# Optimization experiments

Measured on AMD Instinct MI355X. Metric: run time of the kernel, lower is better.

## Reference

```python
import jax, jax.numpy as jnp
import numpy as np


def _gcn_conv(x, W, b, src, dst, num_nodes):
    """PyG GCNConv: linear transform, add self-loops, symmetric norm, scatter-add."""
    h = x @ W  # [N, out] - transform first (cheaper gather on small dim)
    loop = jnp.arange(num_nodes, dtype=src.dtype)
    s = jnp.concatenate([src, loop])  # sources (message senders)
    d = jnp.concatenate([dst, loop])  # targets (aggregators)
    deg = jax.ops.segment_sum(jnp.ones_like(d, dtype=h.dtype), d, num_segments=num_nodes)
    dinv = jnp.where(deg > 0, jax.lax.rsqrt(deg), 0.0)
    norm = dinv[s] * dinv[d]  # [E+N]
    msg = h[s] * norm[:, None]  # gather + scale
    out = jax.ops.segment_sum(msg, d, num_segments=num_nodes)  # scatter-add
    return out + b


def setup_inputs() -> dict:
    key = jax.random.key(0)
    k1, k2, k3, k4 = jax.random.split(key, 4)
    N, F_IN, H, C, E = 100000, 128, 16, 7, 3200000
    x = jax.random.normal(k1, (N, F_IN), dtype=jnp.float32)
    edge_index = jax.random.randint(k2, (2, E), 0, N, dtype=jnp.int64)
    W1 = jax.random.normal(k3, (F_IN, H), dtype=jnp.float32) / np.sqrt(F_IN)
    b1 = jnp.zeros((H,), dtype=jnp.float32)
    W2 = jax.random.normal(k4, (H, C), dtype=jnp.float32) / np.sqrt(H)
    b2 = jnp.zeros((C,), dtype=jnp.float32)
    return {"x": x, "edge_index": edge_index, "W1": W1, "b1": b1, "W2": W2, "b2": b2}


def reference(x, edge_index, W1, b1, W2, b2):
    N = x.shape[0]
    src, dst = edge_index[0], edge_index[1]
    h = _gcn_conv(x, W1, b1, src, dst, N)
    h = jax.nn.relu(h)
    # dropout is identity in eval mode
    h = _gcn_conv(h, W2, b2, src, dst, N)
    return jax.nn.log_softmax(h, axis=1)
```

## Files before the change

kernel.cpp:

```cpp
#include <hip/hip_runtime.h>

#define BSHIFT 7
#define BNODES 128
#define BMASK 127
#define CAP 6144
#define PT 512
#define P_EPB (PT * 16)
#define TPB 256

__device__ __forceinline__ unsigned pkbf2(float a, float b) {
    unsigned ua = __float_as_uint(a), ub = __float_as_uint(b);
    ua = (ua + 0x7fffu + ((ua >> 16) & 1u)) >> 16;
    ub = (ub + 0x7fffu + ((ub >> 16) & 1u)) >> 16;
    return ua | (ub << 16);
}
__device__ __forceinline__ float bflo(unsigned u) { return __uint_as_float(u << 16); }
__device__ __forceinline__ float bfhi(unsigned u) { return __uint_as_float(u & 0xffff0000u); }

__global__ void detect_kernel(const unsigned int* __restrict__ w, int* __restrict__ flag,
                              int* __restrict__ gcur, int nb) {
    __shared__ int any;
    if (threadIdx.x == 0) any = 0;
    __syncthreads();
    int nz = 0;
    for (int k = threadIdx.x; k < 1024; k += blockDim.x)
        if (w[2 * k + 1] != 0u) nz = 1;
    if (nz) atomicOr(&any, 1);
    for (int i = threadIdx.x; i < nb; i += blockDim.x) gcur[i] = 0;
    __syncthreads();
    if (threadIdx.x == 0) *flag = (any == 0) ? 1 : 0;
}

__global__ __launch_bounds__(PT) void fused_place_gemm_kernel(
    const void* __restrict__ ei, const int* __restrict__ flag,
    int* __restrict__ gcur, unsigned* __restrict__ pairs,
    const float* __restrict__ x, const float* __restrict__ W1,
    float* __restrict__ hs, int E, int nb, int pb, int N) {
    __shared__ alignas(16) char smem[47120];
    int tid = threadIdx.x;
    if ((int)blockIdx.x < pb) {
        int* cnt  = (int*)smem;
        int* bbs  = (int*)(smem + 4096);
        int* cur  = (int*)(smem + 8208);
        int* ssum = (int*)(smem + 12304);
        unsigned* stage = (unsigned*)(smem + 14352);
        const bool is64 = (*flag != 0);
        const long long* e64 = (const long long*)ei;
        const int* e32 = (const int*)ei;
        int e0 = blockIdx.x * P_EPB;
        int tot = E - e0; if (tot > P_EPB) tot = P_EPB;
        for (int b = tid; b < nb; b += PT) cnt[b] = 0;
        __syncthreads();
        unsigned pk[16];
        int bk[16];
#pragma unroll
        for (int k = 0; k < 16; ++k) {
            int i = tid + k * PT;
            bk[k] = -1;
            if (i < tot) {
                int e = e0 + i;
                int s, d;
                if (is64) { s = (int)e64[e]; d = (int)e64[E + e]; }
                else      { s = e32[e];      d = e32[E + e]; }
                int b = d >> BSHIFT;
                bk[k] = b;
                pk[k] = ((unsigned)s << BSHIFT) | (unsigned)(d & BMASK);
                atomicAdd(&cnt[b], 1);
            }
        }
        __syncthreads();
        int t2 = tid * 2;
        int c0 = (t2 < nb) ? cnt[t2] : 0;
        int c1 = (t2 + 1 < nb) ? cnt[t2 + 1] : 0;
        int ts = c0 + c1;
        ssum[tid] = ts;
        __syncthreads();
        for (int off = 1; off < PT; off <<= 1) {
            int v = (tid >= off) ? ssum[tid - off] : 0;
            __syncthreads();
            ssum[tid] += v;
            __syncthreads();
        }
        int excl = ssum[tid] - ts;
        if (tid == PT - 1) bbs[nb] = ssum[PT - 1];
        int gb0 = 0, gb1 = 0;
        if (t2 < nb && c0) gb0 = atomicAdd(&gcur[t2], c0);
        if (t2 + 1 < nb && c1) gb1 = atomicAdd(&gcur[t2 + 1], c1);
        if (t2 < nb)     { bbs[t2] = excl;          cnt[t2] = gb0;     cur[t2] = 0; }
        if (t2 + 1 < nb) { bbs[t2 + 1] = excl + c0; cnt[t2 + 1] = gb1; cur[t2 + 1] = 0; }
        __syncthreads();
#pragma unroll
        for (int k = 0; k < 16; ++k) {
            if (bk[k] >= 0) {
                int r = atomicAdd(&cur[bk[k]], 1);
                stage[bbs[bk[k]] + r] = pk[k];
            }
        }
        __syncthreads();
        for (int i = tid; i < tot; i += PT) {
            int lo = 0, hi = nb;
            while (hi - lo > 1) { int mid = (lo + hi) >> 1; if (bbs[mid] <= i) lo = mid; else hi = mid; }
            int slot = cnt[lo] + (i - bbs[lo]);
            if (slot < CAP) pairs[(size_t)lo * CAP + slot] = stage[i];
        }
    } else {
        float* Ws = (float*)smem;
        for (int i = tid; i < 2048; i += PT) Ws[i] = W1[i];
        __syncthreads();
        int n = ((int)blockIdx.x - pb) * PT + tid;
        if (n >= N) return;
        const float4* xp = (const float4*)(x + (size_t)n * 128);
        float a[16];
#pragma unroll
        for (int j = 0; j < 16; ++j) a[j] = 0.f;
#pragma unroll 4
        for (int k4 = 0; k4 < 32; ++k4) {
            float4 xv = xp[k4];
            const float* wr = &Ws[k4 * 64];
#pragma unroll
            for (int j = 0; j < 16; ++j) a[j] += xv.x * wr[j];
#pragma unroll
            for (int j = 0; j < 16; ++j) a[j] += xv.y * wr[16 + j];
#pragma unroll
            for (int j = 0; j < 16; ++j) a[j] += xv.z * wr[32 + j];
#pragma unroll
            for (int j = 0; j < 16; ++j) a[j] += xv.w * wr[48 + j];
        }
        float4* hp = (float4*)(hs + (size_t)n * 16);
#pragma unroll
        for (int j4 = 0; j4 < 4; ++j4) {
            float4 v;
            v.x = a[j4 * 4 + 0]; v.y = a[j4 * 4 + 1];
            v.z = a[j4 * 4 + 2]; v.w = a[j4 * 4 + 3];
            hp[j4] = v;
        }
    }
}

__global__ __launch_bounds__(1024) void scanb_kernel(const int* __restrict__ gcur,
                                                     int* __restrict__ bbase, int nb) {
    __shared__ int sh[1024];
    int t = threadIdx.x;
    int v = 0;
    if (t < nb) { v = gcur[t]; if (v > CAP) v = CAP; }
    sh[t] = v;
    __syncthreads();
    for (int off = 1; off < 1024; off <<= 1) {
        int u = (t >= off) ? sh[t - off] : 0;
        __syncthreads();
        sh[t] += u;
        __syncthreads();
    }
    if (t < nb) bbase[t] = sh[t] - v;
}

__global__ __launch_bounds__(TPB) void csr_build_kernel(
    const unsigned* __restrict__ pairs, const int* __restrict__ gcur,
    const int* __restrict__ bbase, int* __restrict__ csr,
    int* __restrict__ row, int* __restrict__ degA,
    const float* __restrict__ hs1f, uint4* __restrict__ hs1b, int N) {
    __shared__ int hist[BNODES];
    __shared__ int sc[BNODES];
    __shared__ int cur[BNODES];
    __shared__ int stage[CAP];
    int tid = threadIdx.x;
    int b = blockIdx.x;
    if (tid < BNODES) hist[tid] = 0;
    __syncthreads();
    int cnt = gcur[b]; if (cnt > CAP) cnt = CAP;
    int base = bbase[b];
    const unsigned* sl = pairs + (size_t)b * CAP;
    for (int i = tid; i < cnt; i += TPB)
        atomicAdd(&hist[sl[i] & BMASK], 1);
    __syncthreads();
    if (tid < BNODES) sc[tid] = hist[tid];
    __syncthreads();
    for (int off = 1; off < BNODES; off <<= 1) {
        int u = (tid < BNODES && tid >= off) ? sc[tid - off] : 0;
        __syncthreads();
        if (tid < BNODES) sc[tid] += u;
        __syncthreads();
    }
    if (tid < BNODES) {
        int excl = sc[tid] - hist[tid];
        sc[tid] = excl;
        cur[tid] = 0;
        int node = (b << BSHIFT) + tid;
        if (node < N) {
            row[node]  = base + excl;
            degA[node] = hist[tid];
        }
    }
    __syncthreads();
    for (int i = tid; i < cnt; i += TPB) {
        unsigned val = sl[i];
        int l = val & BMASK;
        int r = atomicAdd(&cur[l], 1);
        stage[sc[l] + r] = (int)(val >> BSHIFT);
    }
    __syncthreads();
    for (int i = tid; i < cnt; i += TPB)
        csr[base + i] = stage[i];
    int nodeBase = b << BSHIFT;
    {
        int ln = tid >> 1, half = tid & 1;
        int node = nodeBase + ln;
        if (node < N) {
            float s = rsqrtf((float)(hist[ln] + 1));
            const float4* F = (const float4*)(hs1f + (size_t)node * 16);
            float4 f0 = F[half * 2], f1 = F[half * 2 + 1];
            uint4 u;
            u.x = pkbf2(f0.x * s, f0.y * s); u.y = pkbf2(f0.z * s, f0.w * s);
            u.z = pkbf2(f1.x * s, f1.y * s); u.w = pkbf2(f1.z * s, f1.w * s);
            hs1b[(size_t)node * 2 + half] = u;
        }
    }
}

__global__ __launch_bounds__(TPB) void agg1_kernel(
    const uint4* __restrict__ hs1b, const int* __restrict__ csr,
    const int* __restrict__ row, const int* __restrict__ degA,
    const float* __restrict__ W2, const float* __restrict__ b1,
    uint4* __restrict__ hs2b, int N) {
    __shared__ float Ws[112];
    __shared__ float bs[16];
    int tid = threadIdx.x;
    if (tid < 112) Ws[tid] = W2[tid];
    if (tid < 16) bs[tid] = b1[tid];
    __syncthreads();
    int g = blockIdx.x * TPB + tid;
    int n = g >> 2, quarter = g & 3;
    int st = 0, cnt = 0;
    if (n < N) { st = row[n]; cnt = degA[n]; }
    float acc[16];
#pragma unroll
    for (int j = 0; j < 16; ++j) acc[j] = 0.f;
    int i = st + quarter, end = st + cnt;
    for (; i + 4 < end; i += 8) {
        int s0 = csr[i], s1 = csr[i + 4];
        uint4 g0 = hs1b[(size_t)s0 * 2], g1 = hs1b[(size_t)s0 * 2 + 1];
        uint4 h0 = hs1b[(size_t)s1 * 2], h1 = hs1b[(size_t)s1 * 2 + 1];
        acc[0]  += bflo(g0.x) + bflo(h0.x); acc[1]  += bfhi(g0.x) + bfhi(h0.x);
        acc[2]  += bflo(g0.y) + bflo(h0.y); acc[3]  += bfhi(g0.y) + bfhi(h0.y);
        acc[4]  += bflo(g0.z) + bflo(h0.z); acc[5]  += bfhi(g0.z) + bfhi(h0.z);
        acc[6]  += bflo(g0.w) + bflo(h0.w); acc[7]  += bfhi(g0.w) + bfhi(h0.w);
        acc[8]  += bflo(g1.x) + bflo(h1.x); acc[9]  += bfhi(g1.x) + bfhi(h1.x);
        acc[10] += bflo(g1.y) + bflo(h1.y); acc[11] += bfhi(g1.y) + bfhi(h1.y);
        acc[12] += bflo(g1.z) + bflo(h1.z); acc[13] += bfhi(g1.z) + bfhi(h1.z);
        acc[14] += bflo(g1.w) + bflo(h1.w); acc[15] += bfhi(g1.w) + bfhi(h1.w);
    }
    if (i < end) {
        int s0 = csr[i];
        uint4 g0 = hs1b[(size_t)s0 * 2], g1 = hs1b[(size_t)s0 * 2 + 1];
        acc[0]  += bflo(g0.x); acc[1]  += bfhi(g0.x);
        acc[2]  += bflo(g0.y); acc[3]  += bfhi(g0.y);
        acc[4]  += bflo(g0.z); acc[5]  += bfhi(g0.z);
        acc[6]  += bflo(g0.w); acc[7]  += bfhi(g0.w);
        acc[8]  += bflo(g1.x); acc[9]  += bfhi(g1.x);
        acc[10] += bflo(g1.y); acc[11] += bfhi(g1.y);
        acc[12] += bflo(g1.z); acc[13] += bfhi(g1.z);
        acc[14] += bflo(g1.w); acc[15] += bfhi(g1.w);
    }
#pragma unroll
    for (int j = 0; j < 16; ++j) {
        acc[j] += __shfl_xor(acc[j], 1);
        acc[j] += __shfl_xor(acc[j], 2);
    }
    if (quarter == 0 && n < N) {
        float sc = rsqrtf((float)(cnt + 1));
        uint4 sA = hs1b[(size_t)n * 2], sB = hs1b[(size_t)n * 2 + 1];
        float self[16] = {bflo(sA.x), bfhi(sA.x), bflo(sA.y), bfhi(sA.y),
                          bflo(sA.z), bfhi(sA.z), bflo(sA.w), bfhi(sA.w),
                          bflo(sB.x), bfhi(sB.x), bflo(sB.y), bfhi(sB.y),
                          bflo(sB.z), bfhi(sB.z), bflo(sB.w), bfhi(sB.w)};
        float v[16];
#pragma unroll
        for (int j = 0; j < 16; ++j)
            v[j] = fmaxf(0.f, sc * (acc[j] + self[j]) + bs[j]);
        float h[7];
#pragma unroll
        for (int j = 0; j < 7; ++j) h[j] = 0.f;
#pragma unroll
        for (int k = 0; k < 16; ++k)
#pragma unroll
            for (int j = 0; j < 7; ++j) h[j] += v[k] * Ws[k * 7 + j];
        uint4 u;
        u.x = pkbf2(h[0] * sc, h[1] * sc);
        u.y = pkbf2(h[2] * sc, h[3] * sc);
        u.z = pkbf2(h[4] * sc, h[5] * sc);
        u.w = pkbf2(h[6] * sc, 0.f);
        hs2b[n] = u;
    }
}

__global__ __launch_bounds__(TPB) void agg2_kernel(
    const uint4* __restrict__ hs2b, const int* __restrict__ csr,
    const int* __restrict__ row, const int* __restrict__ degA,
    const float* __restrict__ b2, float* __restrict__ out, int N) {
    __shared__ float bs[8];
    if (threadIdx.x < 7) bs[threadIdx.x] = b2[threadIdx.x];
    __syncthreads();
    int g = blockIdx.x * TPB + threadIdx.x;
    int n = g >> 2, quarter = g & 3;
    int st = 0, cnt = 0;
    if (n < N) { st = row[n]; cnt = degA[n]; }
    float acc[7];
#pragma unroll
    for (int j = 0; j < 7; ++j) acc[j] = 0.f;
    int i = st + quarter, end = st + cnt;
    for (; i + 4 < end; i += 8) {
        int s0 = csr[i], s1 = csr[i + 4];
        uint4 q = hs2b[s0];
        uint4 r = hs2b[s1];
        acc[0] += bflo(q.x) + bflo(r.x); acc[1] += bfhi(q.x) + bfhi(r.x);
        acc[2] += bflo(q.y) + bflo(r.y); acc[3] += bfhi(q.y) + bfhi(r.y);
        acc[4] += bflo(q.z) + bflo(r.z); acc[5] += bfhi(q.z) + bfhi(r.z);
        acc[6] += bflo(q.w) + bflo(r.w);
    }
    if (i < end) {
        uint4 q = hs2b[csr[i]];
        acc[0] += bflo(q.x); acc[1] += bfhi(q.x);
        acc[2] += bflo(q.y); acc[3] += bfhi(q.y);
        acc[4] += bflo(q.z); acc[5] += bfhi(q.z);
        acc[6] += bflo(q.w);
    }
#pragma unroll
    for (int j = 0; j < 7; ++j) {
        acc[j] += __shfl_xor(acc[j], 1);
        acc[j] += __shfl_xor(acc[j], 2);
    }
    if (quarter == 0 && n < N) {
        float sc = rsqrtf((float)(cnt + 1));
        uint4 q = hs2b[n];
        float self[7] = {bflo(q.x), bfhi(q.x), bflo(q.y), bfhi(q.y),
                         bflo(q.z), bfhi(q.z), bflo(q.w)};
        float v[7];
#pragma unroll
        for (int j = 0; j < 7; ++j)
            v[j] = sc * (acc[j] + self[j]) + bs[j];
        float m = v[0];
#pragma unroll
        for (int j = 1; j < 7; ++j) m = fmaxf(m, v[j]);
        float ssum = 0.f;
#pragma unroll
        for (int j = 0; j < 7; ++j) ssum += __expf(v[j] - m);
        float l = m + __logf(ssum);
        float* op = out + (size_t)n * 7;
#pragma unroll
        for (int j = 0; j < 7; ++j) op[j] = v[j] - l;
    }
}

extern "C" void kernel_launch(void* const* d_in, const int* in_sizes, int n_in,
                              void* d_out, int out_size, void* d_ws, size_t ws_size,
                              hipStream_t stream) {
    const float* x  = (const float*)d_in[0];
    const void*  ei = d_in[1];
    const float* W1 = (const float*)d_in[2];
    const float* b1 = (const float*)d_in[3];
    const float* W2 = (const float*)d_in[4];
    const float* b2 = (const float*)d_in[5];
    float* out = (float*)d_out;

    const int Hh  = in_sizes[3];
    const int Fin = in_sizes[2] / Hh;
    const int N   = in_sizes[0] / Fin;
    const long long twoE = in_sizes[1];
    const int E = (int)(twoE / 2);
    const int nb = (N + BNODES - 1) >> BSHIFT;
    (void)n_in; (void)out_size; (void)ws_size;

    char* p = (char*)d_ws;
    auto alloc = [&](size_t bytes) {
        char* r = p;
        p += (bytes + 63) & ~(size_t)63;
        return r;
    };
    int*      flag  = (int*)alloc(sizeof(int));
    int*      gcur  = (int*)alloc(sizeof(int) * (size_t)nb);
    int*      bbase = (int*)alloc(sizeof(int) * 1024);
    unsigned* pairs = (unsigned*)alloc(sizeof(unsigned) * (size_t)nb * CAP);
    int*      csr   = (int*)alloc(sizeof(int) * (size_t)E);
    int*      rowA  = (int*)alloc(sizeof(int) * (size_t)N);
    int*      degA  = (int*)alloc(sizeof(int) * (size_t)N);
    float*    hs1f  = (float*)alloc(sizeof(float) * (size_t)N * 16);
    uint4*    hs1b  = (uint4*)alloc(32 * (size_t)N);
    uint4*    hs2b  = (uint4*)alloc(16 * (size_t)N);

    const int pb = (E + P_EPB - 1) / P_EPB;
    const int gb = (N + PT - 1) / PT;

    detect_kernel<<<1, 256, 0, stream>>>((const unsigned int*)ei, flag, gcur, nb);
    fused_place_gemm_kernel<<<pb + gb, PT, 0, stream>>>(
        ei, flag, gcur, pairs, x, W1, hs1f, E, nb, pb, N);
    scanb_kernel<<<1, 1024, 0, stream>>>(gcur, bbase, nb);
    csr_build_kernel<<<nb, TPB, 0, stream>>>(pairs, gcur, bbase, csr, rowA, degA, hs1f, hs1b, N);
    int aggBlk = (4 * N + TPB - 1) / TPB;
    agg1_kernel<<<aggBlk, TPB, 0, stream>>>(hs1b, csr, rowA, degA, W2, b1, hs2b, N);
    agg2_kernel<<<aggBlk, TPB, 0, stream>>>(hs2b, csr, rowA, degA, b2, out, N);
}
```

Before: 119.7 us.

## Drop bucket scan kernel, store GEMM output as bf16, use 8 lanes per node

Removes the single-block scan kernel by giving each CSR bucket a fixed CAP-sized slot (base = b*CAP), so the scan launch and its serialization go away. The first GEMM now writes bf16-packed outputs instead of fp32, which halves that intermediate's write and read traffic. The normalization step then re-rounds to bf16, adding a second rounding. Both aggregation kernels use 8 threads per node instead of 4, with one more shuffle stage, to expose more memory parallelism per node.

```diff
diff --git a/kernel.cpp b/kernel.cpp
--- a/kernel.cpp
+++ b/kernel.cpp
@@ -35,7 +35,7 @@
     const void* __restrict__ ei, const int* __restrict__ flag,
     int* __restrict__ gcur, unsigned* __restrict__ pairs,
     const float* __restrict__ x, const float* __restrict__ W1,
-    float* __restrict__ hs, int E, int nb, int pb, int N) {
+    uint4* __restrict__ hs1u, int E, int nb, int pb, int N) {
     __shared__ alignas(16) char smem[47120];
     int tid = threadIdx.x;
     if ((int)blockIdx.x < pb) {
@@ -126,39 +126,20 @@
 #pragma unroll
             for (int j = 0; j < 16; ++j) a[j] += xv.w * wr[48 + j];
         }
-        float4* hp = (float4*)(hs + (size_t)n * 16);
-#pragma unroll
-        for (int j4 = 0; j4 < 4; ++j4) {
-            float4 v;
-            v.x = a[j4 * 4 + 0]; v.y = a[j4 * 4 + 1];
-            v.z = a[j4 * 4 + 2]; v.w = a[j4 * 4 + 3];
-            hp[j4] = v;
-        }
-    }
-}
-
-__global__ __launch_bounds__(1024) void scanb_kernel(const int* __restrict__ gcur,
-                                                     int* __restrict__ bbase, int nb) {
-    __shared__ int sh[1024];
-    int t = threadIdx.x;
-    int v = 0;
-    if (t < nb) { v = gcur[t]; if (v > CAP) v = CAP; }
-    sh[t] = v;
-    __syncthreads();
-    for (int off = 1; off < 1024; off <<= 1) {
-        int u = (t >= off) ? sh[t - off] : 0;
-        __syncthreads();
-        sh[t] += u;
-        __syncthreads();
-    }
-    if (t < nb) bbase[t] = sh[t] - v;
+        uint4 u0, u1;
+        u0.x = pkbf2(a[0], a[1]);   u0.y = pkbf2(a[2], a[3]);
+        u0.z = pkbf2(a[4], a[5]);   u0.w = pkbf2(a[6], a[7]);
+        u1.x = pkbf2(a[8], a[9]);   u1.y = pkbf2(a[10], a[11]);
+        u1.z = pkbf2(a[12], a[13]); u1.w = pkbf2(a[14], a[15]);
+        hs1u[(size_t)n * 2]     = u0;
+        hs1u[(size_t)n * 2 + 1] = u1;
+    }
 }
 
 __global__ __launch_bounds__(TPB) void csr_build_kernel(
     const unsigned* __restrict__ pairs, const int* __restrict__ gcur,
-    const int* __restrict__ bbase, int* __restrict__ csr,
-    int* __restrict__ row, int* __restrict__ degA,
-    const float* __restrict__ hs1f, uint4* __restrict__ hs1b, int N) {
+    int* __restrict__ csr, int* __restrict__ row, int* __restrict__ degA,
+    const uint4* __restrict__ hs1u, uint4* __restrict__ hs1b, int N) {
     __shared__ int hist[BNODES];
     __shared__ int sc[BNODES];
     __shared__ int cur[BNODES];
@@ -168,7 +149,7 @@
     if (tid < BNODES) hist[tid] = 0;
     __syncthreads();
     int cnt = gcur[b]; if (cnt > CAP) cnt = CAP;
-    int base = bbase[b];
+    int base = b * CAP;
     const unsigned* sl = pairs + (size_t)b * CAP;
     for (int i = tid; i < cnt; i += TPB)
         atomicAdd(&hist[sl[i] & BMASK], 1);
@@ -201,18 +182,18 @@
     __syncthreads();
     for (int i = tid; i < cnt; i += TPB)
         csr[base + i] = stage[i];
-    int nodeBase = b << BSHIFT;
     {
         int ln = tid >> 1, half = tid & 1;
-        int node = nodeBase + ln;
+        int node = (b << BSHIFT) + ln;
         if (node < N) {
             float s = rsqrtf((float)(hist[ln] + 1));
-            const float4* F = (const float4*)(hs1f + (size_t)node * 16);
-            float4 f0 = F[half * 2], f1 = F[half * 2 + 1];
-            uint4 u;
-            u.x = pkbf2(f0.x * s, f0.y * s); u.y = pkbf2(f0.z * s, f0.w * s);
-            u.z = pkbf2(f1.x * s, f1.y * s); u.w = pkbf2(f1.z * s, f1.w * s);
-            hs1b[(size_t)node * 2 + half] = u;
+            uint4 uu = hs1u[(size_t)node * 2 + half];
+            uint4 o;
+            o.x = pkbf2(bflo(uu.x) * s, bfhi(uu.x) * s);
+            o.y = pkbf2(bflo(uu.y) * s, bfhi(uu.y) * s);
+            o.z = pkbf2(bflo(uu.z) * s, bfhi(uu.z) * s);
+            o.w = pkbf2(bflo(uu.w) * s, bfhi(uu.w) * s);
+            hs1b[(size_t)node * 2 + half] = o;
         }
     }
 }
@@ -229,15 +210,15 @@
     if (tid < 16) bs[tid] = b1[tid];
     __syncthreads();
     int g = blockIdx.x * TPB + tid;
-    int n = g >> 2, quarter = g & 3;
+    int n = g >> 3, oct = g & 7;
     int st = 0, cnt = 0;
     if (n < N) { st = row[n]; cnt = degA[n]; }
     float acc[16];
 #pragma unroll
     for (int j = 0; j < 16; ++j) acc[j] = 0.f;
-    int i = st + quarter, end = st + cnt;
-    for (; i + 4 < end; i += 8) {
-        int s0 = csr[i], s1 = csr[i + 4];
+    int i = st + oct, end = st + cnt;
+    for (; i + 8 < end; i += 16) {
+        int s0 = csr[i], s1 = csr[i + 8];
         uint4 g0 = hs1b[(size_t)s0 * 2], g1 = hs1b[(size_t)s0 * 2 + 1];
         uint4 h0 = hs1b[(size_t)s1 * 2], h1 = hs1b[(size_t)s1 * 2 + 1];
         acc[0]  += bflo(g0.x) + bflo(h0.x); acc[1]  += bfhi(g0.x) + bfhi(h0.x);
@@ -265,8 +246,9 @@
     for (int j = 0; j < 16; ++j) {
         acc[j] += __shfl_xor(acc[j], 1);
         acc[j] += __shfl_xor(acc[j], 2);
-    }
-    if (quarter == 0 && n < N) {
+        acc[j] += __shfl_xor(acc[j], 4);
+    }
+    if (oct == 0 && n < N) {
         float sc = rsqrtf((float)(cnt + 1));
         uint4 sA = hs1b[(size_t)n * 2], sB = hs1b[(size_t)n * 2 + 1];
         float self[16] = {bflo(sA.x), bfhi(sA.x), bflo(sA.y), bfhi(sA.y),
@@ -301,15 +283,15 @@
     if (threadIdx.x < 7) bs[threadIdx.x] = b2[threadIdx.x];
     __syncthreads();
     int g = blockIdx.x * TPB + threadIdx.x;
-    int n = g >> 2, quarter = g & 3;
+    int n = g >> 3, oct = g & 7;
     int st = 0, cnt = 0;
     if (n < N) { st = row[n]; cnt = degA[n]; }
     float acc[7];
 #pragma unroll
     for (int j = 0; j < 7; ++j) acc[j] = 0.f;
-    int i = st + quarter, end = st + cnt;
-    for (; i + 4 < end; i += 8) {
-        int s0 = csr[i], s1 = csr[i + 4];
+    int i = st + oct, end = st + cnt;
+    for (; i + 8 < end; i += 16) {
+        int s0 = csr[i], s1 = csr[i + 8];
         uint4 q = hs2b[s0];
         uint4 r = hs2b[s1];
         acc[0] += bflo(q.x) + bflo(r.x); acc[1] += bfhi(q.x) + bfhi(r.x);
@@ -328,8 +310,9 @@
     for (int j = 0; j < 7; ++j) {
         acc[j] += __shfl_xor(acc[j], 1);
         acc[j] += __shfl_xor(acc[j], 2);
-    }
-    if (quarter == 0 && n < N) {
+        acc[j] += __shfl_xor(acc[j], 4);
+    }
+    if (oct == 0 && n < N) {
         float sc = rsqrtf((float)(cnt + 1));
         uint4 q = hs2b[n];
         float self[7] = {bflo(q.x), bfhi(q.x), bflo(q.y), bfhi(q.y),
@@ -378,12 +361,11 @@
     };
     int*      flag  = (int*)alloc(sizeof(int));
     int*      gcur  = (int*)alloc(sizeof(int) * (size_t)nb);
-    int*      bbase = (int*)alloc(sizeof(int) * 1024);
     unsigned* pairs = (unsigned*)alloc(sizeof(unsigned) * (size_t)nb * CAP);
-    int*      csr   = (int*)alloc(sizeof(int) * (size_t)E);
+    int*      csr   = (int*)alloc(sizeof(int) * (size_t)nb * CAP);
     int*      rowA  = (int*)alloc(sizeof(int) * (size_t)N);
     int*      degA  = (int*)alloc(sizeof(int) * (size_t)N);
-    float*    hs1f  = (float*)alloc(sizeof(float) * (size_t)N * 16);
+    uint4*    hs1u  = (uint4*)alloc(32 * (size_t)N);
     uint4*    hs1b  = (uint4*)alloc(32 * (size_t)N);
     uint4*    hs2b  = (uint4*)alloc(16 * (size_t)N);
 
@@ -392,10 +374,8 @@
 
     detect_kernel<<<1, 256, 0, stream>>>((const unsigned int*)ei, flag, gcur, nb);
     fused_place_gemm_kernel<<<pb + gb, PT, 0, stream>>>(
-        ei, flag, gcur, pairs, x, W1, hs1f, E, nb, pb, N);
-    scanb_kernel<<<1, 1024, 0, stream>>>(gcur, bbase, nb);
-    csr_build_kernel<<<nb, TPB, 0, stream>>>(pairs, gcur, bbase, csr, rowA, degA, hs1f, hs1b, N);
-    int aggBlk = (4 * N + TPB - 1) / TPB;
-    agg1_kernel<<<aggBlk, TPB, 0, stream>>>(hs1b, csr, rowA, degA, W2, b1, hs2b, N);
-    agg2_kernel<<<aggBlk, TPB, 0, stream>>>(hs2b, csr, rowA, degA, b2, out, N);
-}
+        ei, flag, gcur, pairs, x, W1, hs1u, E, nb, pb, N);
+    csr_build_kernel<<<nb, TPB, 0, stream>>>(pairs, gcur, csr, rowA, degA, hs1u, hs1b, N);
+    agg1_kernel<<<(8 * N + TPB - 1) / TPB, TPB, 0, stream>>>(hs1b, csr, rowA, degA, W2, b1, hs2b, N);
+    agg2_kernel<<<(8 * N + TPB - 1) / TPB, TPB, 0, stream>>>(hs2b, csr, rowA, degA, b2, out, N);
+}
```

Result: faster. 113.1 us (-5.5%).
